# Kernel optimization log

Hardware: AMD Instinct MI355X
Metric: run time of the kernel (lower is better)

Reference implementation:

```python
import jax, jax.numpy as jnp
import numpy as np

N, C_IN, H, W = 16, 32, 512, 512
C_OUT, K, STRIDE = 32, 3, 1


def setup_inputs() -> dict:
    key = jax.random.key(0)
    k1, k2, k3 = jax.random.split(key, 3)
    x = jax.random.normal(k1, (N, C_IN, H, W), dtype=jnp.float32)
    weight = jax.random.normal(k2, (C_OUT, C_IN, K, K), dtype=jnp.float32) * 0.05
    bias = jax.random.normal(k3, (C_OUT,), dtype=jnp.float32) * 0.05
    return {"x": x, "weight": weight, "bias": bias}


def reference(x, weight, bias):
    # Direct 2D convolution, NCHW / OIHW, stride 1, no padding (VALID),
    # matching the module's per-pixel multiply+sum with padding=0.
    out = jax.lax.conv_general_dilated(
        x, weight,
        window_strides=(STRIDE, STRIDE),
        padding="VALID",
        dimension_numbers=("NCHW", "OIHW", "NCHW"),
    )
    return out + bias[None, :, None, None]
```

## Files before the change

### kernel.cpp

```cpp
#include <hip/hip_runtime.h>


namespace {
constexpr int NI    = 16;
constexpr int C_IN  = 32;
constexpr int HI    = 512;
constexpr int WI    = 512;
constexpr int C_OUT = 32;
constexpr int HO    = 510;
constexpr int WO    = 510;

constexpr int RT    = 6;
constexpr int PT    = 512;
constexpr int XCOLS = 514;
constexpr int PSTR  = 40;
constexpr int SLOTS = 3;
constexpr int SLOTW = XCOLS * PSTR;
constexpr int LDS_BYTES = SLOTS * SLOTW * 2;
constexpr int HIWI  = HI * WI;
constexpr int NT    = 1024;
}

typedef __attribute__((ext_vector_type(4))) float  floatx4;
typedef __attribute__((ext_vector_type(8))) __bf16 bf16x8;
typedef __attribute__((ext_vector_type(8))) unsigned short ushortx8;

__global__ void conv_wprep(const float* __restrict__ w, __bf16* __restrict__ ws) {
  const int t = threadIdx.x;
  for (int i = t; i < 9 * 2 * 64 * 8; i += 256) {
    const int j    = i & 7;
    const int lane = (i >> 3) & 63;
    const int h    = (i >> 9) & 1;
    const int tap  = i >> 10;
    const int co   = h * 16 + (lane & 15);
    const int ci   = (lane >> 4) * 8 + j;
    ws[i] = (__bf16)w[(co * C_IN + ci) * 9 + tap];
  }
}

__global__ __launch_bounds__(NT, 4)
void conv3x3_mfma(const float* __restrict__ x, const __bf16* __restrict__ ws,
                  const float* __restrict__ bias, float* __restrict__ out) {
  extern __shared__ __bf16 lds[];

  const int t    = threadIdx.x;
  const int lane = t & 63;
  const int wv   = t >> 6;
  const int quad = lane >> 4;
  const int l16  = lane & 15;
  const int ch   = wv >> 3;
  const int w8   = wv & 7;

  const int y0 = blockIdx.x * RT;
  const int n  = blockIdx.y;

  const float* xn = x + (size_t)n * C_IN * HIWI;

  const int ps   = t & 511;
  const int cq   = t >> 9;
  const int gofs = (cq * 16) * HIWI + ps;
  const int lofs = ps * PSTR + cq * 16;

  auto issue = [&](int gr, float (&b)[16]) {
    const float* rb = xn + (size_t)(y0 + gr) * WI;
#pragma unroll
    for (int k = 0; k < 16; ++k) b[k] = rb[gofs + k * HIWI];
  };
  auto commit = [&](int slot, float (&b)[16]) {
    __bf16* s = lds + slot * SLOTW + lofs;
    union { __bf16 bb[16]; ushortx8 u[2]; } pk;
#pragma unroll
    for (int k = 0; k < 16; ++k) pk.bb[k] = (__bf16)b[k];
    *reinterpret_cast<ushortx8*>(s)     = pk.u[0];
    *reinterpret_cast<ushortx8*>(s + 8) = pk.u[1];
  };

  {
    float p0[16], p1[16], p2[16];
    issue(0, p0); issue(1, p1); issue(2, p2);
    commit(0, p0); commit(1, p1); commit(2, p2);
  }

  bf16x8 afrag[9];
#pragma unroll
  for (int tap = 0; tap < 9; ++tap)
    afrag[tap] = *reinterpret_cast<const bf16x8*>(ws + ((tap * 2 + ch) * 64 + lane) * 8);

  float bv[4];
#pragma unroll
  for (int r = 0; r < 4; ++r)
    bv[r] = bias[ch * 16 + quad * 4 + r];

  __syncthreads();

  const int pxb = w8 * 64 + l16;
  floatx4 acc[3][4];
  float buf[16];

#pragma unroll
  for (int ir = 0; ir < RT + 2; ++ir) {
    if (ir + 3 <= RT + 1) issue(ir + 3, buf);

    if (ir < RT) {
#pragma unroll
      for (int f = 0; f < 4; ++f)
        acc[ir % 3][f] = floatx4{bv[0], bv[1], bv[2], bv[3]};
    }

    const __bf16* sl = lds + (ir % SLOTS) * SLOTW + (w8 * 64 + l16) * PSTR + quad * 8;
#pragma unroll
    for (int kx = 0; kx < 3; ++kx) {
      bf16x8 bfr[4];
#pragma unroll
      for (int f = 0; f < 4; ++f)
        bfr[f] = *reinterpret_cast<const bf16x8*>(sl + (f * 16 + kx) * PSTR);
#pragma unroll
      for (int ky = 0; ky < 3; ++ky) {
        const int o = ir - ky;
        if (o < 0 || o >= RT) continue;
#pragma unroll
        for (int f = 0; f < 4; ++f)
          acc[o % 3][f] = __builtin_amdgcn_mfma_f32_16x16x32_bf16(
              afrag[ky * 3 + kx], bfr[f], acc[o % 3][f], 0, 0, 0);
      }
    }

    if (ir >= 2) {
      const int o = ir - 2;
      float* op = out + ((size_t)(n * C_OUT + ch * 16 + quad * 4) * HO + (y0 + o)) * WO + pxb;
#pragma unroll
      for (int f = 0; f < 4; ++f) {
        if (pxb + f * 16 < WO) {
#pragma unroll
          for (int r = 0; r < 4; ++r)
            op[r * (HO * WO) + f * 16] = acc[o % 3][f][r];
        }
      }
    }

    __syncthreads();
    if (ir + 3 <= RT + 1)
      commit(ir % SLOTS, buf);
  }
}

extern "C" void kernel_launch(void* const* d_in, const int* in_sizes, int n_in,
                              void* d_out, int out_size, void* d_ws, size_t ws_size,
                              hipStream_t stream) {
  const float* x    = (const float*)d_in[0];
  const float* w    = (const float*)d_in[1];
  const float* bias = (const float*)d_in[2];
  float* out        = (float*)d_out;
  __bf16* ws        = (__bf16*)d_ws;

  static bool lds_cfg = false;
  if (!lds_cfg) {
    hipFuncSetAttribute((const void*)conv3x3_mfma,
                        hipFuncAttributeMaxDynamicSharedMemorySize, LDS_BYTES);
    lds_cfg = true;
  }

  conv_wprep<<<dim3(1), 256, 0, stream>>>(w, ws);

  dim3 grid(HO / RT, NI);
  conv3x3_mfma<<<grid, NT, LDS_BYTES, stream>>>(x, ws, bias, out);
}
```

Before: 976.9 us.

## Compute output rows one at a time, remap blocks across XCDs, pin waves per EU

The main loop now iterates over output rows and reads three LDS slots per row, instead of iterating over input rows and accumulating into three rotating output accumulators. This cuts accumulator register pressure, but it loads B fragments from LDS three times as often and adds a second barrier per iteration. Block indices are also remapped so that consecutive blocks, which are likely spread round-robin across XCDs, cover contiguous row ranges of the same image, aiming for better L2 locality. Occupancy is pinned with amdgpu_waves_per_eu(4,4) in place of the min-blocks launch bound.

```diff
diff --git a/kernel.cpp b/kernel.cpp
--- a/kernel.cpp
+++ b/kernel.cpp
@@ -11,7 +11,6 @@
 constexpr int WO    = 510;
 
 constexpr int RT    = 6;
-constexpr int PT    = 512;
 constexpr int XCOLS = 514;
 constexpr int PSTR  = 40;
 constexpr int SLOTS = 3;
@@ -38,7 +37,8 @@
   }
 }
 
-__global__ __launch_bounds__(NT, 4)
+__global__ __launch_bounds__(NT)
+__attribute__((amdgpu_waves_per_eu(4, 4)))
 void conv3x3_mfma(const float* __restrict__ x, const __bf16* __restrict__ ws,
                   const float* __restrict__ bias, float* __restrict__ out) {
   extern __shared__ __bf16 lds[];
@@ -51,8 +51,10 @@
   const int ch   = wv >> 3;
   const int w8   = wv & 7;
 
-  const int y0 = blockIdx.x * RT;
-  const int n  = blockIdx.y;
+  const int L   = blockIdx.x + 85 * blockIdx.y;
+  const int wid = (L & 7) * 170 + (L >> 3);
+  const int y0  = (wid % 85) * RT;
+  const int n   = wid / 85;
 
   const float* xn = x + (size_t)n * C_IN * HIWI;
 
@@ -94,53 +96,48 @@
   __syncthreads();
 
   const int pxb = w8 * 64 + l16;
-  floatx4 acc[3][4];
   float buf[16];
 
 #pragma unroll
-  for (int ir = 0; ir < RT + 2; ++ir) {
-    if (ir + 3 <= RT + 1) issue(ir + 3, buf);
+  for (int o = 0; o < RT; ++o) {
+    if (o + 3 <= RT + 1) issue(o + 3, buf);
 
-    if (ir < RT) {
+    floatx4 acc[4];
 #pragma unroll
-      for (int f = 0; f < 4; ++f)
-        acc[ir % 3][f] = floatx4{bv[0], bv[1], bv[2], bv[3]};
-    }
+    for (int f = 0; f < 4; ++f)
+      acc[f] = floatx4{bv[0], bv[1], bv[2], bv[3]};
 
-    const __bf16* sl = lds + (ir % SLOTS) * SLOTW + (w8 * 64 + l16) * PSTR + quad * 8;
 #pragma unroll
-    for (int kx = 0; kx < 3; ++kx) {
-      bf16x8 bfr[4];
+    for (int ky = 0; ky < 3; ++ky) {
+      const __bf16* sl = lds + ((o + ky) % SLOTS) * SLOTW
+                       + (w8 * 64 + l16) * PSTR + quad * 8;
 #pragma unroll
-      for (int f = 0; f < 4; ++f)
-        bfr[f] = *reinterpret_cast<const bf16x8*>(sl + (f * 16 + kx) * PSTR);
-#pragma unroll
-      for (int ky = 0; ky < 3; ++ky) {
-        const int o = ir - ky;
-        if (o < 0 || o >= RT) continue;
+      for (int kx = 0; kx < 3; ++kx) {
+        bf16x8 bfr[4];
 #pragma unroll
         for (int f = 0; f < 4; ++f)
-          acc[o % 3][f] = __builtin_amdgcn_mfma_f32_16x16x32_bf16(
-              afrag[ky * 3 + kx], bfr[f], acc[o % 3][f], 0, 0, 0);
+          bfr[f] = *reinterpret_cast<const bf16x8*>(sl + (f * 16 + kx) * PSTR);
+#pragma unroll
+        for (int f = 0; f < 4; ++f)
+          acc[f] = __builtin_amdgcn_mfma_f32_16x16x32_bf16(
+              afrag[ky * 3 + kx], bfr[f], acc[f], 0, 0, 0);
       }
     }
 
-    if (ir >= 2) {
-      const int o = ir - 2;
-      float* op = out + ((size_t)(n * C_OUT + ch * 16 + quad * 4) * HO + (y0 + o)) * WO + pxb;
+    float* op = out + ((size_t)(n * C_OUT + ch * 16 + quad * 4) * HO + (y0 + o)) * WO + pxb;
 #pragma unroll
-      for (int f = 0; f < 4; ++f) {
-        if (pxb + f * 16 < WO) {
+    for (int f = 0; f < 4; ++f) {
+      if (pxb + f * 16 < WO) {
 #pragma unroll
-          for (int r = 0; r < 4; ++r)
-            op[r * (HO * WO) + f * 16] = acc[o % 3][f][r];
-        }
+        for (int r = 0; r < 4; ++r)
+          op[r * (HO * WO) + f * 16] = acc[f][r];
       }
     }
 
     __syncthreads();
-    if (ir + 3 <= RT + 1)
-      commit(ir % SLOTS, buf);
+    if (o + 3 <= RT + 1)
+      commit(o % SLOTS, buf);
+    __syncthreads();
   }
 }
 
```

New measurement: 953.0 us. 1.03x faster.
